# Performance work log

Measured on AMD Instinct MI355X. Metric: run time of the kernel, lower is better.

The kernel has to match this reference:

```python
import jax, jax.numpy as jnp
import numpy as np

LORA_ALPHA = 16.0
TOP_K = 2


def setup_inputs() -> dict:
    key = jax.random.key(0)
    k_x, k_w, k_g, k_a, k_b = jax.random.split(key, 5)
    B, S, H, O, E, R = 2, 2048, 2048, 2048, 8, 16
    x = jax.random.normal(k_x, (B, S, H), dtype=jnp.float32)
    weight = jax.random.normal(k_w, (O, H), dtype=jnp.float32)          # frozen base W [out, in]
    gate_w = jax.random.normal(k_g, (E, H), dtype=jnp.float32) * 0.02   # router gate [E, in]
    A_w = jax.random.normal(k_a, (E, R, H), dtype=jnp.float32) * (1.0 / np.sqrt(H))  # stacked lora_A
    B_w = jax.random.normal(k_b, (E, O, R), dtype=jnp.float32) * 0.01   # stacked lora_B
    return {"x": x, "weight": weight, "gate_w": gate_w, "A_w": A_w, "B_w": B_w}


def reference(x, weight, gate_w, A_w, B_w):
    E = gate_w.shape[0]
    # Base frozen linear: F.linear(x, weight)
    out = jnp.einsum("bsh,oh->bso", x, weight)

    # Router: softmax over experts, top-2, renormalize
    logits = jnp.einsum("bsh,eh->bse", x, gate_w)
    probs = jax.nn.softmax(logits, axis=-1)
    topk_w, topk_idx = jax.lax.top_k(probs, TOP_K)          # [b,s,2]
    topk_w = topk_w / jnp.sum(topk_w, axis=-1, keepdims=True)

    # Per-token combine weight for each expert (sum over the 2 slots)
    onehot = jax.nn.one_hot(topk_idx, E, dtype=x.dtype)      # [b,s,2,E]
    cw = jnp.einsum("bsk,bske->bse", topk_w, onehot)         # [b,s,E]

    # LoRA: down-project into all experts' rank spaces, weight, then up-project.
    # t: [b,s,E,r] is small (r=16); weighting here avoids a [b,s,E,out] buffer.
    t = jnp.einsum("bsh,erh->bser", x, A_w)
    t = t * cw[..., None]
    lora = jnp.einsum("bser,eor->bso", t, B_w)

    return out + LORA_ALPHA * lora
```

## Files before the change

kernel.cpp:

```cpp
#include <hip/hip_runtime.h>
#include <hip/hip_bf16.h>


typedef __bf16 bf16x8 __attribute__((ext_vector_type(8)));
typedef float f32x4 __attribute__((ext_vector_type(4)));

__device__ __forceinline__ __bf16 f2bf(float f) { return (__bf16)f; }

__device__ __forceinline__ void ld_lds16(const void* g, void* l) {
  __builtin_amdgcn_global_load_lds((__attribute__((address_space(1))) void*)g,
                                   (__attribute__((address_space(3))) void*)l,
                                   16, 0, 0);
}

__global__ void prep_kernel(const float* __restrict__ W, const float* __restrict__ Aw,
                            const float* __restrict__ Bw, __bf16* __restrict__ Bfull,
                            __bf16* __restrict__ A2) {
  const int b = blockIdx.x, tid = threadIdx.x;
  if (b < 2176) {
    const float* src = (b < 2048) ? (W + (size_t)b * 2048)
                                  : (Aw + (size_t)(b - 2048) * 2048);
    __bf16* dst = (b < 2048) ? (Bfull + (size_t)b * 2176)
                             : (A2 + (size_t)(b - 2048) * 2048);
    const int c = tid * 8;
    float4 a = *(const float4*)(src + c);
    float4 d = *(const float4*)(src + c + 4);
    bf16x8 v;
    v[0] = f2bf(a.x); v[1] = f2bf(a.y); v[2] = f2bf(a.z); v[3] = f2bf(a.w);
    v[4] = f2bf(d.x); v[5] = f2bf(d.y); v[6] = f2bf(d.z); v[7] = f2bf(d.w);
    *(bf16x8*)(dst + c) = v;
  } else {
    const int idx = (b - 2176) * 256 + tid;
    const int e = idx >> 11, o = idx & 2047;
    const float4* s = (const float4*)(Bw + ((size_t)e * 2048 + o) * 16);
    float4 v0 = s[0], v1 = s[1], v2 = s[2], v3 = s[3];
    __bf16* d = Bfull + (size_t)o * 2176 + 2048 + e * 16;
    bf16x8 lo, hi;
    lo[0] = f2bf(v0.x); lo[1] = f2bf(v0.y); lo[2] = f2bf(v0.z); lo[3] = f2bf(v0.w);
    lo[4] = f2bf(v1.x); lo[5] = f2bf(v1.y); lo[6] = f2bf(v1.z); lo[7] = f2bf(v1.w);
    hi[0] = f2bf(v2.x); hi[1] = f2bf(v2.y); hi[2] = f2bf(v2.z); hi[3] = f2bf(v2.w);
    hi[4] = f2bf(v3.x); hi[5] = f2bf(v3.y); hi[6] = f2bf(v3.z); hi[7] = f2bf(v3.w);
    *(bf16x8*)d = lo;
    *(bf16x8*)(d + 8) = hi;
  }
}

__global__ __launch_bounds__(256) void router_t2(
    const float* __restrict__ x, const float* __restrict__ gw,
    const __bf16* __restrict__ A2, __bf16* __restrict__ Abuf) {
  __shared__ __align__(16) __bf16 xs[16][2056];
  __shared__ float red[4][16][8];
  __shared__ float cws[16][8];
  const int tid = threadIdx.x;
  const int wave = tid >> 6, lane = tid & 63;
  const int t0 = blockIdx.x * 16;

#pragma unroll 4
  for (int i = 0; i < 16; ++i) {
    const float* xr = x + (size_t)(t0 + i) * 2048 + tid * 8;
    float4 a = *(const float4*)xr;
    float4 b = *(const float4*)(xr + 4);
    bf16x8 v;
    v[0] = f2bf(a.x); v[1] = f2bf(a.y); v[2] = f2bf(a.z); v[3] = f2bf(a.w);
    v[4] = f2bf(b.x); v[5] = f2bf(b.y); v[6] = f2bf(b.z); v[7] = f2bf(b.w);
    *(bf16x8*)(Abuf + (size_t)(t0 + i) * 2176 + tid * 8) = v;
    *(bf16x8*)&xs[i][tid * 8] = v;
  }
  __syncthreads();

  const int tok = tid & 15, slc = tid >> 4;
  const int c0 = slc * 128;
  float acc[8] = {0, 0, 0, 0, 0, 0, 0, 0};
  for (int j8 = 0; j8 < 16; ++j8) {
    bf16x8 xv = *(const bf16x8*)&xs[tok][c0 + j8 * 8];
    float xf[8];
#pragma unroll
    for (int j = 0; j < 8; ++j) xf[j] = (float)xv[j];
#pragma unroll
    for (int e = 0; e < 8; ++e) {
      float4 g0 = *(const float4*)(gw + e * 2048 + c0 + j8 * 8);
      float4 g1 = *(const float4*)(gw + e * 2048 + c0 + j8 * 8 + 4);
      acc[e] += xf[0] * g0.x + xf[1] * g0.y + xf[2] * g0.z + xf[3] * g0.w +
                xf[4] * g1.x + xf[5] * g1.y + xf[6] * g1.z + xf[7] * g1.w;
    }
  }
#pragma unroll
  for (int e = 0; e < 8; ++e) {
    acc[e] += __shfl_down(acc[e], 16);
    acc[e] += __shfl_down(acc[e], 32);
  }
  if (lane < 16) {
#pragma unroll
    for (int e = 0; e < 8; ++e) red[wave][lane][e] = acc[e];
  }
  __syncthreads();
  if (tid < 16) {
    float lg[8];
#pragma unroll
    for (int e = 0; e < 8; ++e)
      lg[e] = red[0][tid][e] + red[1][tid][e] + red[2][tid][e] + red[3][tid][e];
    int a = 0;
    for (int e = 1; e < 8; ++e) if (lg[e] > lg[a]) a = e;
    int b = (a == 0) ? 1 : 0;
    for (int e = 0; e < 8; ++e) if (e != a && lg[e] > lg[b]) b = e;
    const float d = __expf(lg[b] - lg[a]);
    float o[8] = {0, 0, 0, 0, 0, 0, 0, 0};
    o[a] = 1.0f / (1.0f + d);
    o[b] = d / (1.0f + d);
#pragma unroll
    for (int e = 0; e < 8; ++e) cws[tid][e] = o[e];
  }
  __syncthreads();

  const int m = lane & 15, q = lane >> 4;
  const int nt0 = wave * 2;
  f32x4 tacc[2] = {};
  for (int ks = 0; ks < 64; ++ks) {
    bf16x8 af = *(const bf16x8*)&xs[m][ks * 32 + q * 8];
#pragma unroll
    for (int h = 0; h < 2; ++h) {
      bf16x8 bfg = *(const bf16x8*)(A2 + (size_t)((nt0 + h) * 16 + m) * 2048 +
                                    ks * 32 + q * 8);
      tacc[h] = __builtin_amdgcn_mfma_f32_16x16x32_bf16(af, bfg, tacc[h], 0, 0, 0);
    }
  }
#pragma unroll
  for (int h = 0; h < 2; ++h) {
    const int nt = nt0 + h;
#pragma unroll
    for (int rg = 0; rg < 4; ++rg) {
      const int trow = q * 4 + rg;
      const float s = tacc[h][rg] * 16.0f * cws[trow][nt];
      Abuf[(size_t)(t0 + trow) * 2176 + 2048 + nt * 16 + m] = f2bf(s);
    }
  }
}

__global__ __launch_bounds__(256, 2) void mfma_gemm_bt4(
    const __bf16* __restrict__ A, const __bf16* __restrict__ B,
    float* __restrict__ C, int lda, int ldb, int ldc, int kiters) {
  __shared__ __align__(16) __bf16 lds[2 * 16384];
  const int tid = threadIdx.x;
  const int wave = tid >> 6;
  const int lane = tid & 63;

  const int wg = blockIdx.x + (blockIdx.y << 5);
  const int xcd = wg & 7, loc = wg >> 3;
  const int tm = ((xcd & 3) * 8 + (loc >> 3)) * 128;
  const int tn = ((xcd >> 2) * 8 + (loc & 7)) * 128;

  const int srow = lane >> 3;
  const int skoff = ((lane & 7) ^ srow) * 8;

  const int wr = wave >> 1, wc = wave & 1;
  const int rlo = lane & 7;
  const int rb3 = (lane >> 3) & 1;
  const int qb = lane >> 4;

  f32x4 acc[4][4] = {};

  auto stage = [&](int buf, int kt) {
    const int kc = kt * 64;
    __bf16* Ls = lds + buf * 16384;
#pragma unroll
    for (int r = 0; r < 4; ++r) {
      const int ch = wave + r * 4;
      ld_lds16(A + (size_t)(tm + ch * 8 + srow) * lda + kc + skoff, &Ls[ch * 512]);
    }
#pragma unroll
    for (int r = 0; r < 4; ++r) {
      const int ch = wave + r * 4;
      ld_lds16(B + (size_t)(tn + ch * 8 + srow) * ldb + kc + skoff,
               &Ls[8192 + ch * 512]);
    }
  };

  stage(0, 0);

  for (int kt = 0; kt < kiters; ++kt) {
    const int cb = kt & 1;
    if (kt + 1 < kiters) {
      stage(cb ^ 1, kt + 1);
      asm volatile("s_waitcnt vmcnt(8)" ::: "memory");
    } else {
      asm volatile("s_waitcnt vmcnt(0)" ::: "memory");
    }
    __builtin_amdgcn_s_barrier();

    const __bf16* As = lds + cb * 16384;
    const __bf16* Bs = As + 8192;
#pragma unroll
    for (int ks = 0; ks < 2; ++ks) {
      bf16x8 af[4], bfg[4];
      const int q8 = ((ks * 4 + qb) ^ rlo) * 8;
#pragma unroll
      for (int i = 0; i < 4; ++i) {
        const int rh = wr * 8 + i * 2 + rb3;
        af[i] = *(const bf16x8*)&As[rh * 512 + rlo * 64 + q8];
      }
#pragma unroll
      for (int j = 0; j < 4; ++j) {
        const int rh = wc * 8 + j * 2 + rb3;
        bfg[j] = *(const bf16x8*)&Bs[rh * 512 + rlo * 64 + q8];
      }
      __builtin_amdgcn_s_setprio(1);
#pragma unroll
      for (int i = 0; i < 4; ++i)
#pragma unroll
        for (int j = 0; j < 4; ++j)
          acc[i][j] =
              __builtin_amdgcn_mfma_f32_16x16x32_bf16(af[i], bfg[j], acc[i][j], 0, 0, 0);
      __builtin_amdgcn_s_setprio(0);
    }
    __builtin_amdgcn_s_barrier();
  }

  const int crow0 = tm + wr * 64 + (lane >> 4) * 4;
  const int ccol0 = tn + wc * 64 + (lane & 15);
#pragma unroll
  for (int i = 0; i < 4; ++i)
#pragma unroll
    for (int j = 0; j < 4; ++j)
#pragma unroll
      for (int rg = 0; rg < 4; ++rg)
        C[(size_t)(crow0 + i * 16 + rg) * ldc + ccol0 + j * 16] = acc[i][j][rg];
}

extern "C" void kernel_launch(void* const* d_in, const int* in_sizes, int n_in,
                              void* d_out, int out_size, void* d_ws, size_t ws_size,
                              hipStream_t stream) {
  const float* x = (const float*)d_in[0];
  const float* weight = (const float*)d_in[1];
  const float* gate_w = (const float*)d_in[2];
  const float* A_w = (const float*)d_in[3];
  const float* B_w = (const float*)d_in[4];
  float* out = (float*)d_out;

  char* ws = (char*)d_ws;
  __bf16* Abuf = (__bf16*)ws;
  __bf16* Bfull = (__bf16*)(ws + 17825792);
  __bf16* A2 = (__bf16*)(ws + 26738688);

  prep_kernel<<<2240, 256, 0, stream>>>(weight, A_w, B_w, Bfull, A2);
  router_t2<<<256, 256, 0, stream>>>(x, gate_w, A2, Abuf);
  mfma_gemm_bt4<<<dim3(32, 16), 256, 0, stream>>>(Abuf, Bfull, out, 2176, 2176,
                                                  2048, 34);
}
```

Measured before the change: 159.7 us.

## Fuse router logits and x conversion into prep kernel, split LoRA down-projection

```diff
diff --git a/kernel.cpp b/kernel.cpp
--- a/kernel.cpp
+++ b/kernel.cpp
@@ -13,15 +13,67 @@
                                    16, 0, 0);
 }
 
-__global__ void prep_kernel(const float* __restrict__ W, const float* __restrict__ Aw,
-                            const float* __restrict__ Bw, __bf16* __restrict__ Bfull,
-                            __bf16* __restrict__ A2) {
+__global__ __launch_bounds__(256) void prep_logits(
+    const float* __restrict__ x, const float* __restrict__ gw,
+    const float* __restrict__ W, const float* __restrict__ Aw,
+    const float* __restrict__ Bw, __bf16* __restrict__ Abuf,
+    __bf16* __restrict__ Bfull, __bf16* __restrict__ A2,
+    float* __restrict__ cw) {
   const int b = blockIdx.x, tid = threadIdx.x;
-  if (b < 2176) {
-    const float* src = (b < 2048) ? (W + (size_t)b * 2048)
-                                  : (Aw + (size_t)(b - 2048) * 2048);
-    __bf16* dst = (b < 2048) ? (Bfull + (size_t)b * 2176)
-                             : (A2 + (size_t)(b - 2048) * 2048);
+
+  if (b < 1024) {
+    const int wave = tid >> 6, lane = tid & 63;
+    const int t = b * 4 + wave;
+    const float* xr = x + (size_t)t * 2048;
+    __bf16* ar = Abuf + (size_t)t * 2176;
+    float acc[8] = {0, 0, 0, 0, 0, 0, 0, 0};
+#pragma unroll
+    for (int it = 0; it < 4; ++it) {
+      const int c = it * 512 + lane * 8;
+      float4 a = *(const float4*)(xr + c);
+      float4 d = *(const float4*)(xr + c + 4);
+      bf16x8 v;
+      v[0] = f2bf(a.x); v[1] = f2bf(a.y); v[2] = f2bf(a.z); v[3] = f2bf(a.w);
+      v[4] = f2bf(d.x); v[5] = f2bf(d.y); v[6] = f2bf(d.z); v[7] = f2bf(d.w);
+      *(bf16x8*)(ar + c) = v;
+#pragma unroll
+      for (int e = 0; e < 8; ++e) {
+        float4 g0 = *(const float4*)(gw + e * 2048 + c);
+        float4 g1 = *(const float4*)(gw + e * 2048 + c + 4);
+        acc[e] += a.x * g0.x + a.y * g0.y + a.z * g0.z + a.w * g0.w +
+                  d.x * g1.x + d.y * g1.y + d.z * g1.z + d.w * g1.w;
+      }
+    }
+#pragma unroll
+    for (int e = 0; e < 8; ++e) {
+      acc[e] += __shfl_xor(acc[e], 32);
+      acc[e] += __shfl_xor(acc[e], 16);
+      acc[e] += __shfl_xor(acc[e], 8);
+      acc[e] += __shfl_xor(acc[e], 4);
+      acc[e] += __shfl_xor(acc[e], 2);
+      acc[e] += __shfl_xor(acc[e], 1);
+    }
+    if (lane == 0) {
+      int a_ = 0;
+      for (int e = 1; e < 8; ++e) if (acc[e] > acc[a_]) a_ = e;
+      int b_ = (a_ == 0) ? 1 : 0;
+      for (int e = 0; e < 8; ++e) if (e != a_ && acc[e] > acc[b_]) b_ = e;
+      const float d = __expf(acc[b_] - acc[a_]);
+      float o[8] = {0, 0, 0, 0, 0, 0, 0, 0};
+      o[a_] = 1.0f / (1.0f + d);
+      o[b_] = d / (1.0f + d);
+      *(float4*)(cw + (size_t)t * 8) = make_float4(o[0], o[1], o[2], o[3]);
+      *(float4*)(cw + (size_t)t * 8 + 4) = make_float4(o[4], o[5], o[6], o[7]);
+    }
+    return;
+  }
+
+  const int pb = b - 1024;
+  if (pb < 2176) {
+    const float* src = (pb < 2048) ? (W + (size_t)pb * 2048)
+                                   : (Aw + (size_t)(pb - 2048) * 2048);
+    __bf16* dst = (pb < 2048) ? (Bfull + (size_t)pb * 2176)
+                              : (A2 + (size_t)(pb - 2048) * 2048);
     const int c = tid * 8;
     float4 a = *(const float4*)(src + c);
     float4 d = *(const float4*)(src + c + 4);
@@ -30,7 +82,7 @@
     v[4] = f2bf(d.x); v[5] = f2bf(d.y); v[6] = f2bf(d.z); v[7] = f2bf(d.w);
     *(bf16x8*)(dst + c) = v;
   } else {
-    const int idx = (b - 2176) * 256 + tid;
+    const int idx = (pb - 2176) * 256 + tid;
     const int e = idx >> 11, o = idx & 2047;
     const float4* s = (const float4*)(Bw + ((size_t)e * 2048 + o) * 16);
     float4 v0 = s[0], v1 = s[1], v2 = s[2], v3 = s[3];
@@ -45,78 +97,18 @@
   }
 }
 
-__global__ __launch_bounds__(256) void router_t2(
-    const float* __restrict__ x, const float* __restrict__ gw,
-    const __bf16* __restrict__ A2, __bf16* __restrict__ Abuf) {
-  __shared__ __align__(16) __bf16 xs[16][2056];
-  __shared__ float red[4][16][8];
-  __shared__ float cws[16][8];
+__global__ __launch_bounds__(256) void lora_t2(
+    const __bf16* __restrict__ Abuf, const __bf16* __restrict__ A2,
+    const float* __restrict__ cw, __bf16* __restrict__ Aout) {
   const int tid = threadIdx.x;
   const int wave = tid >> 6, lane = tid & 63;
   const int t0 = blockIdx.x * 16;
-
-#pragma unroll 4
-  for (int i = 0; i < 16; ++i) {
-    const float* xr = x + (size_t)(t0 + i) * 2048 + tid * 8;
-    float4 a = *(const float4*)xr;
-    float4 b = *(const float4*)(xr + 4);
-    bf16x8 v;
-    v[0] = f2bf(a.x); v[1] = f2bf(a.y); v[2] = f2bf(a.z); v[3] = f2bf(a.w);
-    v[4] = f2bf(b.x); v[5] = f2bf(b.y); v[6] = f2bf(b.z); v[7] = f2bf(b.w);
-    *(bf16x8*)(Abuf + (size_t)(t0 + i) * 2176 + tid * 8) = v;
-    *(bf16x8*)&xs[i][tid * 8] = v;
-  }
-  __syncthreads();
-
-  const int tok = tid & 15, slc = tid >> 4;
-  const int c0 = slc * 128;
-  float acc[8] = {0, 0, 0, 0, 0, 0, 0, 0};
-  for (int j8 = 0; j8 < 16; ++j8) {
-    bf16x8 xv = *(const bf16x8*)&xs[tok][c0 + j8 * 8];
-    float xf[8];
-#pragma unroll
-    for (int j = 0; j < 8; ++j) xf[j] = (float)xv[j];
-#pragma unroll
-    for (int e = 0; e < 8; ++e) {
-      float4 g0 = *(const float4*)(gw + e * 2048 + c0 + j8 * 8);
-      float4 g1 = *(const float4*)(gw + e * 2048 + c0 + j8 * 8 + 4);
-      acc[e] += xf[0] * g0.x + xf[1] * g0.y + xf[2] * g0.z + xf[3] * g0.w +
-                xf[4] * g1.x + xf[5] * g1.y + xf[6] * g1.z + xf[7] * g1.w;
-    }
-  }
-#pragma unroll
-  for (int e = 0; e < 8; ++e) {
-    acc[e] += __shfl_down(acc[e], 16);
-    acc[e] += __shfl_down(acc[e], 32);
-  }
-  if (lane < 16) {
-#pragma unroll
-    for (int e = 0; e < 8; ++e) red[wave][lane][e] = acc[e];
-  }
-  __syncthreads();
-  if (tid < 16) {
-    float lg[8];
-#pragma unroll
-    for (int e = 0; e < 8; ++e)
-      lg[e] = red[0][tid][e] + red[1][tid][e] + red[2][tid][e] + red[3][tid][e];
-    int a = 0;
-    for (int e = 1; e < 8; ++e) if (lg[e] > lg[a]) a = e;
-    int b = (a == 0) ? 1 : 0;
-    for (int e = 0; e < 8; ++e) if (e != a && lg[e] > lg[b]) b = e;
-    const float d = __expf(lg[b] - lg[a]);
-    float o[8] = {0, 0, 0, 0, 0, 0, 0, 0};
-    o[a] = 1.0f / (1.0f + d);
-    o[b] = d / (1.0f + d);
-#pragma unroll
-    for (int e = 0; e < 8; ++e) cws[tid][e] = o[e];
-  }
-  __syncthreads();
-
   const int m = lane & 15, q = lane >> 4;
   const int nt0 = wave * 2;
   f32x4 tacc[2] = {};
+  const __bf16* arow = Abuf + (size_t)(t0 + m) * 2176 + q * 8;
   for (int ks = 0; ks < 64; ++ks) {
-    bf16x8 af = *(const bf16x8*)&xs[m][ks * 32 + q * 8];
+    bf16x8 af = *(const bf16x8*)(arow + ks * 32);
 #pragma unroll
     for (int h = 0; h < 2; ++h) {
       bf16x8 bfg = *(const bf16x8*)(A2 + (size_t)((nt0 + h) * 16 + m) * 2048 +
@@ -130,8 +122,8 @@
 #pragma unroll
     for (int rg = 0; rg < 4; ++rg) {
       const int trow = q * 4 + rg;
-      const float s = tacc[h][rg] * 16.0f * cws[trow][nt];
-      Abuf[(size_t)(t0 + trow) * 2176 + 2048 + nt * 16 + m] = f2bf(s);
+      const float s = tacc[h][rg] * 16.0f * cw[(size_t)(t0 + trow) * 8 + nt];
+      Aout[(size_t)(t0 + trow) * 2176 + 2048 + nt * 16 + m] = f2bf(s);
     }
   }
 }
@@ -240,9 +232,11 @@
   __bf16* Abuf = (__bf16*)ws;
   __bf16* Bfull = (__bf16*)(ws + 17825792);
   __bf16* A2 = (__bf16*)(ws + 26738688);
-
-  prep_kernel<<<2240, 256, 0, stream>>>(weight, A_w, B_w, Bfull, A2);
-  router_t2<<<256, 256, 0, stream>>>(x, gate_w, A2, Abuf);
+  float* cw = (float*)(ws + 27262976);
+
+  prep_logits<<<3264, 256, 0, stream>>>(x, gate_w, weight, A_w, B_w, Abuf, Bfull,
+                                        A2, cw);
+  lora_t2<<<256, 256, 0, stream>>>(Abuf, A2, cw, Abuf);
   mfma_gemm_bt4<<<dim3(32, 16), 256, 0, stream>>>(Abuf, Bfull, out, 2176, 2176,
                                                   2048, 34);
 }
```

Result: slower. 178.7 us (+11.9%).
